# Kernel optimization log

Measured on AMD Instinct MI355X. Metric: run time of the kernel, lower is better.

The kernel has to match this reference:

```python
import jax, jax.numpy as jnp
import numpy as np

OUT_H, OUT_W = 7, 7
SPATIAL_SCALE = 0.25
SAMPLING_RATIO = 2


def setup_inputs() -> dict:
    key = jax.random.key(0)
    kf, kb, kc, ks = jax.random.split(key, 4)
    B, C, H, W = 2, 256, 200, 200
    N, IMG = 1000, 800.0
    features = jax.random.normal(kf, (B, C, H, W), jnp.float32)
    bidx = jax.random.randint(kb, (N,), 0, B).astype(jnp.float32)
    ctr = jax.random.uniform(kc, (N, 2)) * IMG            # box centers in image coords
    size = jax.random.uniform(ks, (N, 2)) * 256.0 + 16.0  # box sizes 16..272 px
    x1y1 = jnp.clip(ctr - size / 2, 0.0, IMG)
    x2y2 = jnp.clip(ctr + size / 2, 0.0, IMG)
    rois = jnp.concatenate(
        [bidx[:, None], x1y1[:, 0:1], x1y1[:, 1:2], x2y2[:, 0:1], x2y2[:, 1:2]], axis=1
    )
    return {"features": features, "rois": rois}


def _roi_align(features, rois):
    # torchvision.ops.roi_align semantics (aligned=False), fully vectorized over ROIs.
    B, C, H, W = features.shape
    N = rois.shape[0]
    ph, pw, ratio, scale = OUT_H, OUT_W, SAMPLING_RATIO, SPATIAL_SCALE
    b = rois[:, 0].astype(jnp.int32)
    x1, y1, x2, y2 = (rois[:, i] * scale for i in (1, 2, 3, 4))
    roi_w = jnp.maximum(x2 - x1, 1.0)
    roi_h = jnp.maximum(y2 - y1, 1.0)
    bin_w = roi_w / pw
    bin_h = roi_h / ph
    # sample coordinate s within bin p: y1 + (p*ratio + i + 0.5) * bin_h / ratio
    sy = jnp.arange(ph * ratio, dtype=features.dtype)
    sx = jnp.arange(pw * ratio, dtype=features.dtype)
    y = y1[:, None] + (sy[None, :] + 0.5) * (bin_h[:, None] / ratio)  # (N, Sy)
    x = x1[:, None] + (sx[None, :] + 0.5) * (bin_w[:, None] / ratio)  # (N, Sx)
    valid = ((y >= -1.0) & (y <= float(H)))[:, :, None] & \
            ((x >= -1.0) & (x <= float(W)))[:, None, :]               # (N, Sy, Sx)
    yc = jnp.clip(y, 0.0, H - 1.0)
    xc = jnp.clip(x, 0.0, W - 1.0)
    y0 = jnp.floor(yc).astype(jnp.int32)
    x0 = jnp.floor(xc).astype(jnp.int32)
    y1i = jnp.minimum(y0 + 1, H - 1)
    x1i = jnp.minimum(x0 + 1, W - 1)
    ly = (yc - y0)[:, :, None, None]  # (N, Sy, 1, 1)
    lx = (xc - x0)[:, None, :, None]  # (N, 1, Sx, 1)
    hy, hx = 1.0 - ly, 1.0 - lx

    def gather(yi, xi):
        # advanced indexing -> (N, Sy, Sx, C)
        return features[b[:, None, None], :, yi[:, :, None], xi[:, None, :]]

    val = (hy * hx * gather(y0, x0) + hy * lx * gather(y0, x1i)
           + ly * hx * gather(y1i, x0) + ly * lx * gather(y1i, x1i))
    val = jnp.where(valid[..., None], val, 0.0)
    val = val.reshape(N, ph, ratio, pw, ratio, C).mean(axis=(2, 4))  # avg sampling points
    return val.transpose(0, 3, 1, 2)  # (N, C, ph, pw)


def reference(features, rois):
    return _roi_align(features, rois)
```

## Files before the change

### kernel.cpp

```cpp
#include <hip/hip_runtime.h>
#include <hip/hip_fp16.h>

#define OUT_H 7
#define OUT_W 7
#define NPOS  49
#define RATIO 2
#define SCALE 0.25f
#define CCH 256
#define FH 200
#define FW 200
#define FHW (FH * FW)
#define LROW 68

struct __align__(16) H8 { __half2 h[4]; };

__device__ __forceinline__ void acc8(float (&a)[8], const H8& v, float w) {
    #pragma unroll
    for (int k = 0; k < 4; ++k) {
        a[2*k]   = fmaf(__low2float(v.h[k]),  w, a[2*k]);
        a[2*k+1] = fmaf(__high2float(v.h[k]), w, a[2*k+1]);
    }
}

__global__ __launch_bounds__(256) void transpose_cp(
    const float* __restrict__ in, __half* __restrict__ outT)
{
    int bid = blockIdx.x;
    int pt   = bid % 625;
    int rest = bid / 625;
    int ct   = rest & 3;
    int b    = rest >> 2;

    __shared__ unsigned short tile[64][66];
    int tid = threadIdx.x;
    int pix0 = pt * 64, c0 = ct * 64;
    int xl = tid & 63;

    const float* src = in + ((size_t)b * CCH + c0) * FHW + pix0;
    #pragma unroll
    for (int k = 0; k < 16; ++k) {
        int cl = (tid >> 6) + 4 * k;
        tile[xl][cl] = __half_as_ushort(__float2half(src[(size_t)cl * FHW + xl]));
    }
    __syncthreads();

    __half* dst = outT + ((size_t)b * FHW + pix0) * CCH + c0;
    #pragma unroll
    for (int j = 0; j < 8; ++j) {
        int idx = tid + 256 * j;
        int pl = idx >> 5;
        int cp = idx & 31;
        *(unsigned int*)((char*)dst + (size_t)pl * (CCH * 2) + 4 * cp) =
            *(const unsigned int*)&tile[pl][2 * cp];
    }
}

__global__ __launch_bounds__(256) void roi_gather_v4(
    const __half* __restrict__ featT,
    const float* __restrict__ rois,
    float* __restrict__ out,
    int N)
{
    int blk = blockIdx.x;
    int n  = blk >> 2;
    int cq = blk & 3;
    int tid = threadIdx.x;
    int wave = tid >> 6, lane = tid & 63;
    int g = lane >> 3;
    int l = lane & 7;

    __shared__ float lds[NPOS * LROW];

    const float* r = rois + (size_t)n * 5;
    int   b  = (int)r[0];
    float x1 = r[1] * SCALE, y1 = r[2] * SCALE;
    float roi_w = fmaxf(r[3] * SCALE - x1, 1.0f);
    float roi_h = fmaxf(r[4] * SCALE - y1, 1.0f);
    float step_x = roi_w * (1.0f / (OUT_W * RATIO));
    float step_y = roi_h * (1.0f / (OUT_H * RATIO));

    const char* base = (const char*)featT + (size_t)b * ((size_t)FHW * CCH * 2);
    const uint32_t laneoff = (uint32_t)(cq * 64 + l * 8) * 2;

    #pragma unroll 1
    for (int rnd = 0; rnd < 2; ++rnd) {
        int p = rnd * 32 + wave * 8 + g;
        if (p < NPOS) {
            int ph = p / OUT_W;
            int pw = p - ph * OUT_W;
            float acc[8];
            #pragma unroll
            for (int k = 0; k < 8; ++k) acc[k] = 0.0f;

            #pragma unroll
            for (int iy = 0; iy < RATIO; ++iy) {
                float yy = y1 + ((float)(ph * RATIO + iy) + 0.5f) * step_y;
                bool  vy = (yy >= -1.0f) && (yy <= (float)FH);
                float yc = fminf(fmaxf(yy, 0.0f), (float)(FH - 1));
                int   yi0 = (int)yc;
                float ly = yc - (float)yi0, hy = 1.0f - ly;
                uint32_t row0  = (uint32_t)yi0 * (FW * CCH * 2);
                uint32_t rstep = (yi0 < FH - 1) ? (FW * CCH * 2) : 0u;

                #pragma unroll
                for (int ix = 0; ix < RATIO; ++ix) {
                    float xx = x1 + ((float)(pw * RATIO + ix) + 0.5f) * step_x;
                    bool  vx = (xx >= -1.0f) && (xx <= (float)FW);
                    float xc = fminf(fmaxf(xx, 0.0f), (float)(FW - 1));
                    int   xi0 = (int)xc;
                    float lx = xc - (float)xi0, hx = 1.0f - lx;
                    uint32_t dx = (xi0 < FW - 1) ? (CCH * 2) : 0u;

                    float vm  = (vy && vx) ? 0.25f : 0.0f;
                    float hyv = hy * vm, lyv = ly * vm;

                    uint32_t o00 = row0 + (uint32_t)xi0 * (CCH * 2) + laneoff;
                    H8 v00 = *(const H8*)(base + o00);
                    H8 v01 = *(const H8*)(base + o00 + dx);
                    H8 v10 = *(const H8*)(base + o00 + rstep);
                    H8 v11 = *(const H8*)(base + o00 + rstep + dx);

                    acc8(acc, v00, hyv * hx);
                    acc8(acc, v01, hyv * lx);
                    acc8(acc, v10, lyv * hx);
                    acc8(acc, v11, lyv * lx);
                }
            }
            float* lp = &lds[p * LROW + l * 8];
            *(float4*)lp       = make_float4(acc[0], acc[1], acc[2], acc[3]);
            *(float4*)(lp + 4) = make_float4(acc[4], acc[5], acc[6], acc[7]);
        }
    }
    __syncthreads();

    float* oblk = out + ((size_t)n * CCH + cq * 64) * NPOS;
    #pragma unroll 1
    for (int o = tid; o < 64 * NPOS; o += 256) {
        int c = o / NPOS;
        int p = o - c * NPOS;
        oblk[o] = lds[p * LROW + c];
    }
}

__global__ __launch_bounds__(256) void roi_align_kernel(
    const float* __restrict__ feat, const float* __restrict__ rois,
    float* __restrict__ out, int N, int C, int H, int W)
{
    int idx = blockIdx.x * blockDim.x + threadIdx.x;
    int total = N * C * OUT_H * OUT_W;
    if (idx >= total) return;
    int pw = idx % OUT_W;
    int ph = (idx / OUT_W) % OUT_H;
    int c  = (idx / (OUT_W * OUT_H)) % C;
    int n  = idx / (OUT_W * OUT_H * C);
    const float* r = rois + (size_t)n * 5;
    int   b  = (int)r[0];
    float x1 = r[1] * SCALE, y1 = r[2] * SCALE;
    float roi_w = fmaxf(r[3] * SCALE - x1, 1.0f);
    float roi_h = fmaxf(r[4] * SCALE - y1, 1.0f);
    float step_y = roi_h * (1.0f / (OUT_H * RATIO));
    float step_x = roi_w * (1.0f / (OUT_W * RATIO));
    const float* fptr = feat + ((size_t)b * C + c) * (size_t)(H * W);
    float acc = 0.0f;
    #pragma unroll
    for (int iy = 0; iy < RATIO; ++iy) {
        float y = y1 + ((float)(ph * RATIO + iy) + 0.5f) * step_y;
        bool vy = (y >= -1.0f) && (y <= (float)H);
        float ycl = fminf(fmaxf(y, 0.0f), (float)(H - 1));
        int y0 = (int)floorf(ycl), y1i = min(y0 + 1, H - 1);
        float ly = ycl - (float)y0, hy = 1.0f - ly;
        #pragma unroll
        for (int ix = 0; ix < RATIO; ++ix) {
            float x = x1 + ((float)(pw * RATIO + ix) + 0.5f) * step_x;
            bool vx = (x >= -1.0f) && (x <= (float)W);
            float xcl = fminf(fmaxf(x, 0.0f), (float)(W - 1));
            int x0 = (int)floorf(xcl), x1i = min(x0 + 1, W - 1);
            float lx = xcl - (float)x0, hx = 1.0f - lx;
            const float* row0 = fptr + (size_t)y0 * W;
            const float* row1 = fptr + (size_t)y1i * W;
            float v = hy * hx * row0[x0] + hy * lx * row0[x1i]
                    + ly * hx * row1[x0] + ly * lx * row1[x1i];
            acc += (vy && vx) ? v : 0.0f;
        }
    }
    out[idx] = acc * (1.0f / (RATIO * RATIO));
}

extern "C" void kernel_launch(void* const* d_in, const int* in_sizes, int n_in,
                              void* d_out, int out_size, void* d_ws, size_t ws_size,
                              hipStream_t stream) {
    const float* feat = (const float*)d_in[0];
    const float* rois = (const float*)d_in[1];
    float* out = (float*)d_out;

    const int N = in_sizes[1] / 5;
    const int B = in_sizes[0] / (CCH * FHW);

    size_t need = (size_t)B * FHW * CCH * sizeof(__half);
    if (ws_size >= need) {
        __half* featT = (__half*)d_ws;
        transpose_cp<<<B * 4 * 625, 256, 0, stream>>>(feat, featT);
        roi_gather_v4<<<4 * N, 256, 0, stream>>>(featT, rois, out, N);
    } else {
        int total = N * CCH * OUT_H * OUT_W;
        roi_align_kernel<<<(total + 255) / 256, 256, 0, stream>>>(
            feat, rois, out, N, CCH, FH, FW);
    }
}
```

Before: 62.86 us.

## Sort ROIs by Morton order, vectorize transpose loads, remap blocks across XCDs

Adds a one-block bitonic sort of ROIs by batch and Morton code of the box center, fused into the transpose launch, so the gather kernel visits spatially nearby ROIs together. The gather blocks are also remapped round-robin across the 8 XCDs to improve L2 locality. The transpose now reads float4 per thread and writes 16-byte rows from a padded LDS tile, and the output uses nontemporal stores. The single sort block is serialized and may lengthen the first kernel, and the permutation buffer needs extra workspace.

Measured after the change: 68.12 us. +8.4%, slower.

```diff
diff --git a/kernel.cpp b/kernel.cpp
--- a/kernel.cpp
+++ b/kernel.cpp
@@ -11,6 +11,7 @@
 #define FW 200
 #define FHW (FH * FW)
 #define LROW 68
+#define TROW 72
 
 struct __align__(16) H8 { __half2 h[4]; };
 
@@ -22,48 +23,107 @@
     }
 }
 
-__global__ __launch_bounds__(256) void transpose_cp(
-    const float* __restrict__ in, __half* __restrict__ outT)
+__device__ __forceinline__ uint32_t part1by1(uint32_t x) {
+    x &= 0xFFu;
+    x = (x | (x << 4)) & 0x0F0Fu;
+    x = (x | (x << 2)) & 0x3333u;
+    x = (x | (x << 1)) & 0x5555u;
+    return x;
+}
+
+__global__ __launch_bounds__(256) void transpose_sort(
+    const float* __restrict__ in, __half* __restrict__ outT,
+    const float* __restrict__ rois, uint32_t* __restrict__ perm,
+    int N, int B)
 {
+    __shared__ __align__(16) char smem[64 * TROW * 2];
     int bid = blockIdx.x;
+    int tid = threadIdx.x;
+
+    if (bid == 0) {
+        uint64_t* keys = (uint64_t*)smem;
+        if (N <= 1024) {
+            for (int i = tid; i < 1024; i += 256) {
+                uint64_t key = ~0ull;
+                if (i < N) {
+                    const float* r = rois + (size_t)i * 5;
+                    int bb = (int)r[0];
+                    float cx = 0.5f * (r[1] + r[3]) * SCALE;
+                    float cy = 0.5f * (r[2] + r[4]) * SCALE;
+                    uint32_t ix = (uint32_t)fminf(fmaxf(cx, 0.f), 255.f);
+                    uint32_t iy = (uint32_t)fminf(fmaxf(cy, 0.f), 255.f);
+                    uint32_t m = (part1by1(iy) << 1) | part1by1(ix) | ((uint32_t)bb << 16);
+                    key = ((uint64_t)m << 32) | (uint32_t)i;
+                }
+                keys[i] = key;
+            }
+            __syncthreads();
+            for (int sz = 2; sz <= 1024; sz <<= 1) {
+                for (int j = sz >> 1; j > 0; j >>= 1) {
+                    for (int i = tid; i < 1024; i += 256) {
+                        int ixj = i ^ j;
+                        if (ixj > i) {
+                            uint64_t a = keys[i], c = keys[ixj];
+                            bool asc = ((i & sz) == 0);
+                            if ((a > c) == asc) { keys[i] = c; keys[ixj] = a; }
+                        }
+                    }
+                    __syncthreads();
+                }
+            }
+            for (int i = tid; i < N; i += 256) perm[i] = (uint32_t)keys[i];
+        } else {
+            for (int i = tid; i < N; i += 256) perm[i] = (uint32_t)i;
+        }
+        return;
+    }
+
+    bid -= 1;
     int pt   = bid % 625;
     int rest = bid / 625;
     int ct   = rest & 3;
     int b    = rest >> 2;
 
-    __shared__ unsigned short tile[64][66];
-    int tid = threadIdx.x;
-    int pix0 = pt * 64, c0 = ct * 64;
-    int xl = tid & 63;
-
-    const float* src = in + ((size_t)b * CCH + c0) * FHW + pix0;
-    #pragma unroll
-    for (int k = 0; k < 16; ++k) {
-        int cl = (tid >> 6) + 4 * k;
-        tile[xl][cl] = __half_as_ushort(__float2half(src[(size_t)cl * FHW + xl]));
+    ushort* T = (ushort*)smem;
+    int px0 = pt * 64, c0 = ct * 64;
+    int c_l = tid >> 2;
+    int pxg = (tid & 3) << 4;
+
+    const float* src = in + ((size_t)b * CCH + c0 + c_l) * FHW + px0 + pxg;
+    #pragma unroll
+    for (int k = 0; k < 4; ++k) {
+        float4 v = *(const float4*)(src + 4 * k);
+        T[(pxg + 4*k + 0) * TROW + c_l] = __half_as_ushort(__float2half(v.x));
+        T[(pxg + 4*k + 1) * TROW + c_l] = __half_as_ushort(__float2half(v.y));
+        T[(pxg + 4*k + 2) * TROW + c_l] = __half_as_ushort(__float2half(v.z));
+        T[(pxg + 4*k + 3) * TROW + c_l] = __half_as_ushort(__float2half(v.w));
     }
     __syncthreads();
 
-    __half* dst = outT + ((size_t)b * FHW + pix0) * CCH + c0;
-    #pragma unroll
-    for (int j = 0; j < 8; ++j) {
-        int idx = tid + 256 * j;
-        int pl = idx >> 5;
-        int cp = idx & 31;
-        *(unsigned int*)((char*)dst + (size_t)pl * (CCH * 2) + 4 * cp) =
-            *(const unsigned int*)&tile[pl][2 * cp];
-    }
-}
-
-__global__ __launch_bounds__(256) void roi_gather_v4(
+    char* dstB = (char*)(outT + ((size_t)b * FHW + px0) * CCH + c0);
+    #pragma unroll
+    for (int j2 = 0; j2 < 2; ++j2) {
+        int unit = tid + 256 * j2;
+        int pl = unit >> 3;
+        int o8 = unit & 7;
+        uint4 val = *(const uint4*)&T[pl * TROW + o8 * 8];
+        *(uint4*)(dstB + (size_t)pl * (CCH * 2) + o8 * 16) = val;
+    }
+}
+
+__global__ __launch_bounds__(256) void roi_gather_v5(
     const __half* __restrict__ featT,
     const float* __restrict__ rois,
+    const uint32_t* __restrict__ perm,
     float* __restrict__ out,
     int N)
 {
-    int blk = blockIdx.x;
-    int n  = blk >> 2;
-    int cq = blk & 3;
+    int nblk = gridDim.x;
+    int wg = (nblk % 8 == 0)
+           ? ((blockIdx.x & 7) * (nblk >> 3) + (blockIdx.x >> 3))
+           : blockIdx.x;
+    int n  = (int)perm[wg >> 2];
+    int cq = wg & 3;
     int tid = threadIdx.x;
     int wave = tid >> 6, lane = tid & 63;
     int g = lane >> 3;
@@ -138,7 +198,7 @@
     for (int o = tid; o < 64 * NPOS; o += 256) {
         int c = o / NPOS;
         int p = o - c * NPOS;
-        oblk[o] = lds[p * LROW + c];
+        __builtin_nontemporal_store(lds[p * LROW + c], &oblk[o]);
     }
 }
 
@@ -196,11 +256,14 @@
     const int N = in_sizes[1] / 5;
     const int B = in_sizes[0] / (CCH * FHW);
 
-    size_t need = (size_t)B * FHW * CCH * sizeof(__half);
+    size_t featTBytes = (size_t)B * FHW * CCH * sizeof(__half);
+    size_t need = featTBytes + (size_t)N * sizeof(uint32_t);
     if (ws_size >= need) {
         __half* featT = (__half*)d_ws;
-        transpose_cp<<<B * 4 * 625, 256, 0, stream>>>(feat, featT);
-        roi_gather_v4<<<4 * N, 256, 0, stream>>>(featT, rois, out, N);
+        uint32_t* perm = (uint32_t*)((char*)d_ws + featTBytes);
+        transpose_sort<<<B * 4 * 625 + 1, 256, 0, stream>>>(
+            feat, featT, rois, perm, N, B);
+        roi_gather_v5<<<4 * N, 256, 0, stream>>>(featT, rois, perm, out, N);
     } else {
         int total = N * CCH * OUT_H * OUT_W;
         roi_align_kernel<<<(total + 255) / 256, 256, 0, stream>>>(
```

## Stream ROI corner pixels into LDS via async global_load_lds with multi-stage pipeline

Applied to the files above, without the earlier changes.

Rewrites the ROI gather kernel so that each wave handles one output position at a time. Corner-pixel channel vectors are staged into LDS through direct global-to-LDS loads in a three-deep software pipeline, with explicit vmcnt waits. Each lane then reduces one channel from LDS. It also sets a launch-bounds occupancy hint and uses nontemporal output stores. The aim is to hide gather latency by overlapping loads with compute, at the cost of more LDS use, hand-tuned waitcnt logic and less per-lane vectorization.

After: 77.95 us. 24.0% more time.

```diff
diff --git a/kernel.cpp b/kernel.cpp
--- a/kernel.cpp
+++ b/kernel.cpp
@@ -10,17 +10,8 @@
 #define FH 200
 #define FW 200
 #define FHW (FH * FW)
-#define LROW 68
-
-struct __align__(16) H8 { __half2 h[4]; };
-
-__device__ __forceinline__ void acc8(float (&a)[8], const H8& v, float w) {
-    #pragma unroll
-    for (int k = 0; k < 4; ++k) {
-        a[2*k]   = fmaf(__low2float(v.h[k]),  w, a[2*k]);
-        a[2*k+1] = fmaf(__high2float(v.h[k]), w, a[2*k+1]);
-    }
-}
+#define PIXB (CCH * 2)
+#define DEPTH 3
 
 __global__ __launch_bounds__(256) void transpose_cp(
     const float* __restrict__ in, __half* __restrict__ outT)
@@ -55,21 +46,27 @@
     }
 }
 
-__global__ __launch_bounds__(256) void roi_gather_v4(
+__device__ __forceinline__ void gload16(const void* g, void* s) {
+    __builtin_amdgcn_global_load_lds(
+        (const __attribute__((address_space(1))) void*)g,
+        (__attribute__((address_space(3))) void*)s, 16, 0, 0);
+}
+
+__global__ __launch_bounds__(256, 4) void roi_gather_v11(
     const __half* __restrict__ featT,
     const float* __restrict__ rois,
     float* __restrict__ out,
     int N)
 {
-    int blk = blockIdx.x;
-    int n  = blk >> 2;
-    int cq = blk & 3;
-    int tid = threadIdx.x;
-    int wave = tid >> 6, lane = tid & 63;
-    int g = lane >> 3;
-    int l = lane & 7;
-
-    __shared__ float lds[NPOS * LROW];
+    int bid = blockIdx.x;
+    int n  = bid >> 2;
+    int cq = bid & 3;
+    int tid  = threadIdx.x;
+    int wv   = tid >> 6;
+    int lane = tid & 63;
+
+    __shared__ __half pix[4][DEPTH][1024];
+    __shared__ float  ldso[NPOS * 65];
 
     const float* r = rois + (size_t)n * 5;
     int   b  = (int)r[0];
@@ -79,57 +76,77 @@
     float step_x = roi_w * (1.0f / (OUT_W * RATIO));
     float step_y = roi_h * (1.0f / (OUT_H * RATIO));
 
-    const char* base = (const char*)featT + (size_t)b * ((size_t)FHW * CCH * 2);
-    const uint32_t laneoff = (uint32_t)(cq * 64 + l * 8) * 2;
-
+    const char* base = (const char*)featT + (size_t)b * ((size_t)FHW * PIXB)
+                     + (uint32_t)cq * 128;
+    const int qa = lane >> 3;
+    const int cc = qa & 3;
+    const uint32_t bq = (uint32_t)(lane & 7) * 16;
+
+    const int nk = ((48 - wv) >> 2) + 1;
+
+    auto corner_off = [&](int p, int s) -> uint32_t {
+        int ph = p / OUT_W, pw = p - (p / OUT_W) * OUT_W;
+        int iy = s >> 1, ix = s & 1;
+        float yy = y1 + ((float)(ph * RATIO + iy) + 0.5f) * step_y;
+        float xx = x1 + ((float)(pw * RATIO + ix) + 0.5f) * step_x;
+        float yc = fminf(fmaxf(yy, 0.0f), (float)(FH - 1));
+        float xc = fminf(fmaxf(xx, 0.0f), (float)(FW - 1));
+        int yi0 = (int)yc, xi0 = (int)xc;
+        uint32_t rw = (uint32_t)(yi0 * FW + xi0) * PIXB;
+        uint32_t dx = (xi0 < FW - 1) ? PIXB : 0u;
+        uint32_t dy = (yi0 < FH - 1) ? (FW * PIXB) : 0u;
+        return rw + ((cc & 1) ? dx : 0u) + ((cc & 2) ? dy : 0u);
+    };
+
+    auto stage = [&](int k) {
+        int p = wv + 4 * k;
+        uint32_t a0 = corner_off(p, qa >> 2);
+        uint32_t a1 = corner_off(p, (qa >> 2) + 2);
+        __half* dst = &pix[wv][k % DEPTH][0];
+        gload16(base + a0 + bq, (void*)dst);
+        gload16(base + a1 + bq, (void*)(dst + 512));
+    };
+
+    auto consume = [&](int k) {
+        int p = wv + 4 * k;
+        int ph = p / OUT_W, pw = p - (p / OUT_W) * OUT_W;
+        const __half* src = &pix[wv][k % DEPTH][0];
+        float acc = 0.0f;
+        #pragma unroll
+        for (int s = 0; s < 4; ++s) {
+            int iy = s >> 1, ix = s & 1;
+            float yy = y1 + ((float)(ph * RATIO + iy) + 0.5f) * step_y;
+            float xx = x1 + ((float)(pw * RATIO + ix) + 0.5f) * step_x;
+            bool  vv = (yy >= -1.0f) && (yy <= (float)FH)
+                    && (xx >= -1.0f) && (xx <= (float)FW);
+            float yc = fminf(fmaxf(yy, 0.0f), (float)(FH - 1));
+            float xc = fminf(fmaxf(xx, 0.0f), (float)(FW - 1));
+            float ly = yc - (float)(int)yc, hy = 1.0f - ly;
+            float lx = xc - (float)(int)xc, hx = 1.0f - lx;
+            float vm = vv ? 0.25f : 0.0f;
+            float w0 = hy * hx * vm, w1 = hy * lx * vm;
+            float w2 = ly * hx * vm, w3 = ly * lx * vm;
+            acc = fmaf(__half2float(src[(s * 4 + 0) * 64 + lane]), w0, acc);
+            acc = fmaf(__half2float(src[(s * 4 + 1) * 64 + lane]), w1, acc);
+            acc = fmaf(__half2float(src[(s * 4 + 2) * 64 + lane]), w2, acc);
+            acc = fmaf(__half2float(src[(s * 4 + 3) * 64 + lane]), w3, acc);
+        }
+        ldso[p * 65 + lane] = acc;
+    };
+
+    stage(0);
+    stage(1);
     #pragma unroll 1
-    for (int rnd = 0; rnd < 2; ++rnd) {
-        int p = rnd * 32 + wave * 8 + g;
-        if (p < NPOS) {
-            int ph = p / OUT_W;
-            int pw = p - ph * OUT_W;
-            float acc[8];
-            #pragma unroll
-            for (int k = 0; k < 8; ++k) acc[k] = 0.0f;
-
-            #pragma unroll
-            for (int iy = 0; iy < RATIO; ++iy) {
-                float yy = y1 + ((float)(ph * RATIO + iy) + 0.5f) * step_y;
-                bool  vy = (yy >= -1.0f) && (yy <= (float)FH);
-                float yc = fminf(fmaxf(yy, 0.0f), (float)(FH - 1));
-                int   yi0 = (int)yc;
-                float ly = yc - (float)yi0, hy = 1.0f - ly;
-                uint32_t row0  = (uint32_t)yi0 * (FW * CCH * 2);
-                uint32_t rstep = (yi0 < FH - 1) ? (FW * CCH * 2) : 0u;
-
-                #pragma unroll
-                for (int ix = 0; ix < RATIO; ++ix) {
-                    float xx = x1 + ((float)(pw * RATIO + ix) + 0.5f) * step_x;
-                    bool  vx = (xx >= -1.0f) && (xx <= (float)FW);
-                    float xc = fminf(fmaxf(xx, 0.0f), (float)(FW - 1));
-                    int   xi0 = (int)xc;
-                    float lx = xc - (float)xi0, hx = 1.0f - lx;
-                    uint32_t dx = (xi0 < FW - 1) ? (CCH * 2) : 0u;
-
-                    float vm  = (vy && vx) ? 0.25f : 0.0f;
-                    float hyv = hy * vm, lyv = ly * vm;
-
-                    uint32_t o00 = row0 + (uint32_t)xi0 * (CCH * 2) + laneoff;
-                    H8 v00 = *(const H8*)(base + o00);
-                    H8 v01 = *(const H8*)(base + o00 + dx);
-                    H8 v10 = *(const H8*)(base + o00 + rstep);
-                    H8 v11 = *(const H8*)(base + o00 + rstep + dx);
-
-                    acc8(acc, v00, hyv * hx);
-                    acc8(acc, v01, hyv * lx);
-                    acc8(acc, v10, lyv * hx);
-                    acc8(acc, v11, lyv * lx);
-                }
-            }
-            float* lp = &lds[p * LROW + l * 8];
-            *(float4*)lp       = make_float4(acc[0], acc[1], acc[2], acc[3]);
-            *(float4*)(lp + 4) = make_float4(acc[4], acc[5], acc[6], acc[7]);
+    for (int k = 0; k < nk; ++k) {
+        if (k + 2 < nk) {
+            stage(k + 2);
+            asm volatile("s_waitcnt vmcnt(4)" ::: "memory");
+        } else if (k + 1 < nk) {
+            asm volatile("s_waitcnt vmcnt(2)" ::: "memory");
+        } else {
+            asm volatile("s_waitcnt vmcnt(0)" ::: "memory");
         }
+        consume(k);
     }
     __syncthreads();
 
@@ -138,7 +155,7 @@
     for (int o = tid; o < 64 * NPOS; o += 256) {
         int c = o / NPOS;
         int p = o - c * NPOS;
-        oblk[o] = lds[p * LROW + c];
+        __builtin_nontemporal_store(ldso[p * 65 + c], &oblk[o]);
     }
 }
 
@@ -200,7 +217,7 @@
     if (ws_size >= need) {
         __half* featT = (__half*)d_ws;
         transpose_cp<<<B * 4 * 625, 256, 0, stream>>>(feat, featT);
-        roi_gather_v4<<<4 * N, 256, 0, stream>>>(featT, rois, out, N);
+        roi_gather_v11<<<4 * N, 256, 0, stream>>>(featT, rois, out, N);
     } else {
         int total = N * CCH * OUT_H * OUT_W;
         roi_align_kernel<<<(total + 255) / 256, 256, 0, stream>>>(
```
